# Kernel optimization log

Hardware: AMD Instinct MI355X
Metric: run time of the kernel (lower is better)

The kernel has to match this reference:

```python
import jax, jax.numpy as jnp
import numpy as np

PI = np.pi

def setup_inputs() -> dict:
    key = jax.random.key(0)
    ks = jax.random.split(key, 8)
    N, D, K, Q = 8192, 8, 64, 16
    return {
        "X": jax.random.normal(ks[0], (N, D), dtype=jnp.float32),
        "z": jax.random.normal(ks[1], (D, K, Q), dtype=jnp.float32),
        "weight": jax.random.uniform(ks[2], (Q,), dtype=jnp.float32) + 0.5,
        "mu": jax.random.uniform(ks[3], (D, Q), dtype=jnp.float32) + 0.5,
        "std": jax.random.uniform(ks[4], (D, Q), dtype=jnp.float32) + 0.5,
        "alpha": jax.random.uniform(ks[5], (K, Q), dtype=jnp.float32) * PI,
        "var_mu_w": 0.5 * jax.random.uniform(ks[6], (D, K, Q), dtype=jnp.float32),
        "var_sigma_w": 0.05 * jax.random.uniform(ks[7], (D, K, Q), dtype=jnp.float32),
    }

def reference(X, z, weight, mu, std, alpha, var_mu_w, var_sigma_w):
    # Faithful translation of vssgp.get_Ephi (Param.transform treated as identity)
    N, D = X.shape
    _, K, Q = z.shape
    two_over_K = 2.0 * weight[None, None, :] / K                 # [1,1,Q]
    mean_p = 1.0 / (mu + 1e-8)                                   # [D,Q]
    std_p = 1.0 / (2.0 * PI * std + 1e-8)                        # [D,Q]
    E_w = mean_p[:, None, :] + std_p[:, None, :] * var_mu_w      # [D,K,Q]
    xbar = 2.0 * PI * (X[:, :, None, None] - z[None])            # [N,D,K,Q]
    phase = jnp.einsum('ndkq,dkq->nkq', xbar, E_w)               # D-reduction
    cos_w = jnp.cos(alpha[None] + phase)                         # [N,K,Q]
    decay = jnp.exp(-0.5 * jnp.einsum(
        'ndkq,dkq->nkq', (std_p[None, :, None, :] * xbar) ** 2, var_sigma_w))
    E_phi = (jnp.sqrt(two_over_K) * decay * cos_w).reshape(N, K * Q)
    cos_2w = jnp.cos(2.0 * alpha[None] + 2.0 * phase)
    E_cos_sq = two_over_K * (0.5 + 0.5 * decay ** 4 * cos_2w)    # [N,K,Q]
    G = E_phi.T @ E_phi                                          # [KQ,KQ]
    diag_new = E_cos_sq.sum(axis=0).reshape(-1)
    G = G - jnp.diag(jnp.diag(G)) + jnp.diag(diag_new)
    return E_phi, G, E_cos_sq
```

## Files before the change

kernel.cpp:

```cpp
#include <hip/hip_runtime.h>

#define TWO_PI 6.2831853071795864769f

typedef float floatx4 __attribute__((ext_vector_type(4)));
typedef float f32x16 __attribute__((ext_vector_type(16)));
typedef __bf16 bf16x8 __attribute__((ext_vector_type(8)));

__device__ __forceinline__ unsigned short f32_to_bf16(float f) {
    unsigned int u = __float_as_uint(f);
    u += 0x7fffu + ((u >> 16) & 1u);
    return (unsigned short)(u >> 16);
}

__device__ __forceinline__ void gload_lds16(const void* g, void* l) {
    __builtin_amdgcn_global_load_lds(
        (__attribute__((address_space(1))) unsigned int*)g,
        (__attribute__((address_space(3))) unsigned int*)l, 16, 0, 0);
}

__global__ __launch_bounds__(256) void k_precompute(
    const float* __restrict__ z, const float* __restrict__ weight,
    const float* __restrict__ mu, const float* __restrict__ stdv,
    const float* __restrict__ alpha, const float* __restrict__ vmw,
    const float* __restrict__ vsw, float* __restrict__ coef,
    float* __restrict__ colsum)
{
    int kq = blockIdx.x * blockDim.x + threadIdx.x;
    if (kq >= 1024) return;
    colsum[kq] = 0.0f;
    int q = kq & 15;
    float w = weight[q];
    float t2k = w * (2.0f / 64.0f);
    float* c = coef + (size_t)kq * 32;
#pragma unroll
    for (int d = 0; d < 8; ++d) {
        float m = mu[d * 16 + q];
        float s = stdv[d * 16 + q];
        float mean_p = 1.0f / (m + 1e-8f);
        float std_p  = 1.0f / (TWO_PI * s + 1e-8f);
        float Ew  = mean_p + std_p * vmw[d * 1024 + kq];
        float sp2 = std_p * TWO_PI;
        c[d]      = TWO_PI * Ew;
        c[8 + d]  = sp2 * sp2 * vsw[d * 1024 + kq];
        c[16 + d] = z[d * 1024 + kq];
    }
    c[24] = alpha[kq];
    c[25] = sqrtf(t2k);
    c[26] = t2k;
}

__global__ __launch_bounds__(256) void k_ephi(
    const float* __restrict__ X, const float* __restrict__ coef,
    float* __restrict__ Ephi, float* __restrict__ Ecos,
    unsigned short* __restrict__ ET, float* __restrict__ colsum, int N)
{
    __shared__ float Xs[64][8];
    __shared__ unsigned short Ebf[64][66];
    __shared__ float red[256];

    const int tid = threadIdx.x;
    const int kq0 = blockIdx.x * 64;
    const int n0  = blockIdx.y * 64;

    for (int i = tid; i < 512; i += 256)
        Xs[i >> 3][i & 7] = X[(size_t)(n0 + (i >> 3)) * 8 + (i & 7)];
    __syncthreads();

    const int kql = tid & 63;
    const int kq  = kq0 + kql;
    const int nb  = (tid >> 6) * 16;

    const float* c = coef + (size_t)kq * 32;
    float Ac[8], u[8], zv[8];
    *(floatx4*)&Ac[0] = *(const floatx4*)(c + 0);
    *(floatx4*)&Ac[4] = *(const floatx4*)(c + 4);
    *(floatx4*)&u[0]  = *(const floatx4*)(c + 8);
    *(floatx4*)&u[4]  = *(const floatx4*)(c + 12);
    *(floatx4*)&zv[0] = *(const floatx4*)(c + 16);
    *(floatx4*)&zv[4] = *(const floatx4*)(c + 20);
    const float alp = c[24], sqw = c[25], t2k = c[26];

    float csum = 0.0f;
#pragma unroll 4
    for (int nl = 0; nl < 16; ++nl) {
        const int n = nb + nl;
        floatx4 xa = *(const floatx4*)&Xs[n][0];
        floatx4 xb = *(const floatx4*)&Xs[n][4];
        float ph = 0.0f, s = 0.0f;
#pragma unroll
        for (int d = 0; d < 4; ++d) {
            float t = xa[d] - zv[d];
            ph = fmaf(Ac[d], t, ph);
            s  = fmaf(u[d], t * t, s);
        }
#pragma unroll
        for (int d = 0; d < 4; ++d) {
            float t = xb[d] - zv[4 + d];
            ph = fmaf(Ac[4 + d], t, ph);
            s  = fmaf(u[4 + d], t * t, s);
        }
        float cw  = __cosf(alp + ph);
        float dec = __expf(-0.5f * s);
        float ep  = sqw * dec * cw;
        float d2  = dec * dec;
        float c2w = fmaf(2.0f * cw, cw, -1.0f);
        float ec  = t2k * fmaf(0.5f * d2 * d2, c2w, 0.5f);
        csum += ec;
        size_t idx = (size_t)(n0 + n) * 1024 + kq;
        Ephi[idx] = ep;
        Ecos[idx] = ec;
        Ebf[kql][n] = f32_to_bf16(ep);
    }
    red[tid] = csum;
    __syncthreads();
    if (tid < 64) {
        float v = red[tid] + red[tid + 64] + red[tid + 128] + red[tid + 192];
        atomicAdd(&colsum[kq0 + tid], v);
    }

    const int rw = tid >> 3;
    const int cw8 = tid & 7;
#pragma unroll
    for (int cc = 0; cc < 2; ++cc) {
        const int row = rw + cc * 32;
        const unsigned short* s8 = &Ebf[row][cw8 * 8];
        uint4 v;
        v.x = (unsigned)s8[0] | ((unsigned)s8[1] << 16);
        v.y = (unsigned)s8[2] | ((unsigned)s8[3] << 16);
        v.z = (unsigned)s8[4] | ((unsigned)s8[5] << 16);
        v.w = (unsigned)s8[6] | ((unsigned)s8[7] << 16);
        *(uint4*)&ET[(size_t)(kq0 + row) * N + n0 + cw8 * 8] = v;
    }
}

__global__ __launch_bounds__(256) void k_gemm(
    const unsigned short* __restrict__ ET, float* __restrict__ Gpart,
    int N, int KQ)
{
    __shared__ unsigned short At[2][128 * 64];
    __shared__ unsigned short Bt[2][128 * 64];

    const int tid  = threadIdx.x;
    const int wave = tid >> 6, lane = tid & 63;
    const int wi = wave >> 1, wj = wave & 1;

    const int bid = blockIdx.x;
    const int zc  = bid & 7;
    const int t8  = bid >> 3;
    const int i0  = (t8 >> 3) * 128;
    const int j0  = (t8 & 7) * 128;
    const int NS = N >> 3;
    const int nbase = zc * NS;
    const int nsteps = NS >> 6;

    const int srow = tid >> 3;
    const int sch  = (tid & 7) ^ (srow & 7);
    const size_t gA = (size_t)(i0 + srow) * N + nbase + sch * 8;
    const size_t gB = (size_t)(j0 + srow) * N + nbase + sch * 8;

    f32x16 acc[2][2] = {};

    auto STAGE = [&](int buf, int noff) {
        unsigned short* la = &At[buf][wave * 512];
        unsigned short* lb = &Bt[buf][wave * 512];
#pragma unroll
        for (int b = 0; b < 4; ++b) {
            gload_lds16(ET + gA + (size_t)(b * 32) * N + noff, la + b * 2048);
            gload_lds16(ET + gB + (size_t)(b * 32) * N + noff, lb + b * 2048);
        }
    };

    STAGE(0, 0);
    asm volatile("s_waitcnt vmcnt(0)" ::: "memory");
    __syncthreads();

    for (int t = 0; t < nsteps; ++t) {
        const int buf = t & 1;
        if (t + 1 < nsteps) STAGE(buf ^ 1, (t + 1) * 64);

        const unsigned short* Ab = &At[buf][0];
        const unsigned short* Bb = &Bt[buf][0];
        bf16x8 a[2][4], b[2][4];
#pragma unroll
        for (int m = 0; m < 2; ++m) {
            const int r = wi * 64 + m * 32 + (lane & 31);
#pragma unroll
            for (int ks = 0; ks < 4; ++ks) {
                const int ch = (ks * 2 + (lane >> 5)) ^ (r & 7);
                a[m][ks] = *(const bf16x8*)&Ab[r * 64 + ch * 8];
            }
        }
#pragma unroll
        for (int n = 0; n < 2; ++n) {
            const int r = wj * 64 + n * 32 + (lane & 31);
#pragma unroll
            for (int ks = 0; ks < 4; ++ks) {
                const int ch = (ks * 2 + (lane >> 5)) ^ (r & 7);
                b[n][ks] = *(const bf16x8*)&Bb[r * 64 + ch * 8];
            }
        }
#pragma unroll
        for (int ks = 0; ks < 4; ++ks)
#pragma unroll
            for (int m = 0; m < 2; ++m)
#pragma unroll
                for (int n = 0; n < 2; ++n)
                    acc[m][n] = __builtin_amdgcn_mfma_f32_32x32x16_bf16(
                        a[m][ks], b[n][ks], acc[m][n], 0, 0, 0);

        asm volatile("s_waitcnt vmcnt(0)" ::: "memory");
        __syncthreads();
    }

    float* Gp = Gpart + (size_t)zc * KQ * KQ;
    const int colb = j0 + wj * 64 + (lane & 31);
    const int rowb = i0 + wi * 64 + 4 * (lane >> 5);
#pragma unroll
    for (int m = 0; m < 2; ++m)
#pragma unroll
        for (int n = 0; n < 2; ++n)
#pragma unroll
            for (int reg = 0; reg < 16; ++reg) {
                const int row = rowb + m * 32 + (reg & 3) + 8 * (reg >> 2);
                Gp[(size_t)row * KQ + colb + n * 32] = acc[m][n][reg];
            }
}

__global__ __launch_bounds__(256) void k_reduce(
    const float* __restrict__ Gpart, const float* __restrict__ colsum,
    float* __restrict__ G, int KQ)
{
    const size_t off = ((size_t)blockIdx.x * 256 + threadIdx.x) * 4;
    const size_t stride = (size_t)KQ * KQ;
    floatx4 s = *(const floatx4*)&Gpart[off];
#pragma unroll
    for (int z = 1; z < 8; ++z)
        s += *(const floatx4*)&Gpart[(size_t)z * stride + off];
    const int row = (int)(off / (size_t)KQ);
    const int c0  = (int)(off % (size_t)KQ);
    if (row >= c0 && row < c0 + 4) s[row - c0] = colsum[row];
    *(floatx4*)&G[off] = s;
}

extern "C" void kernel_launch(void* const* d_in, const int* in_sizes, int n_in,
                              void* d_out, int out_size, void* d_ws, size_t ws_size,
                              hipStream_t stream)
{
    (void)n_in; (void)out_size; (void)ws_size;
    const float* X      = (const float*)d_in[0];
    const float* z      = (const float*)d_in[1];
    const float* weight = (const float*)d_in[2];
    const float* mu     = (const float*)d_in[3];
    const float* stdv   = (const float*)d_in[4];
    const float* alpha  = (const float*)d_in[5];
    const float* vmw    = (const float*)d_in[6];
    const float* vsw    = (const float*)d_in[7];

    const int N  = in_sizes[0] / 8;
    const int KQ = in_sizes[5];

    float* coef   = (float*)d_ws;
    float* colsum = (float*)((char*)d_ws + 131072);
    unsigned short* ET = (unsigned short*)((char*)d_ws + 135168);
    float* Gpart  = (float*)((char*)d_ws + 135168 + (size_t)KQ * N * 2);

    float* Ephi = (float*)d_out;
    float* G    = Ephi + (size_t)N * KQ;
    float* Ecos = G + (size_t)KQ * KQ;

    k_precompute<<<4, 256, 0, stream>>>(z, weight, mu, stdv, alpha, vmw, vsw, coef, colsum);
    k_ephi<<<dim3(KQ / 64, N / 64), 256, 0, stream>>>(X, coef, Ephi, Ecos, ET, colsum, N);
    k_gemm<<<512, 256, 0, stream>>>(ET, Gpart, N, KQ);
    k_reduce<<<(KQ * KQ) / 1024, 256, 0, stream>>>(Gpart, colsum, G, KQ);
}
```

Measured before the change: 148.6 us.

## Fuse coefficient precompute into ephi kernel, replace atomics with partials, prioritize MFMA

Removes the separate precompute kernel launch by having each ephi block compute its 64 columns of coefficients into shared memory. The column-sum atomics are replaced by per-block partial writes, which the reduce kernel sums serially for diagonal entries. MFMA sections in the GEMM are wrapped in s_setprio to raise wave priority. The cost is that coefficient work is recomputed across all 128 row-blocks, and the reduce kernel does a 128-iteration serial loop on diagonal threads.

New measurement: 168.4 us. 13.4% more time.

```diff
diff --git a/kernel.cpp b/kernel.cpp
--- a/kernel.cpp
+++ b/kernel.cpp
@@ -18,42 +18,15 @@
         (__attribute__((address_space(3))) unsigned int*)l, 16, 0, 0);
 }
 
-__global__ __launch_bounds__(256) void k_precompute(
-    const float* __restrict__ z, const float* __restrict__ weight,
-    const float* __restrict__ mu, const float* __restrict__ stdv,
-    const float* __restrict__ alpha, const float* __restrict__ vmw,
-    const float* __restrict__ vsw, float* __restrict__ coef,
-    float* __restrict__ colsum)
-{
-    int kq = blockIdx.x * blockDim.x + threadIdx.x;
-    if (kq >= 1024) return;
-    colsum[kq] = 0.0f;
-    int q = kq & 15;
-    float w = weight[q];
-    float t2k = w * (2.0f / 64.0f);
-    float* c = coef + (size_t)kq * 32;
-#pragma unroll
-    for (int d = 0; d < 8; ++d) {
-        float m = mu[d * 16 + q];
-        float s = stdv[d * 16 + q];
-        float mean_p = 1.0f / (m + 1e-8f);
-        float std_p  = 1.0f / (TWO_PI * s + 1e-8f);
-        float Ew  = mean_p + std_p * vmw[d * 1024 + kq];
-        float sp2 = std_p * TWO_PI;
-        c[d]      = TWO_PI * Ew;
-        c[8 + d]  = sp2 * sp2 * vsw[d * 1024 + kq];
-        c[16 + d] = z[d * 1024 + kq];
-    }
-    c[24] = alpha[kq];
-    c[25] = sqrtf(t2k);
-    c[26] = t2k;
-}
-
 __global__ __launch_bounds__(256) void k_ephi(
-    const float* __restrict__ X, const float* __restrict__ coef,
+    const float* __restrict__ X, const float* __restrict__ zc,
+    const float* __restrict__ weight, const float* __restrict__ mu,
+    const float* __restrict__ stdv, const float* __restrict__ alpha,
+    const float* __restrict__ vmw, const float* __restrict__ vsw,
     float* __restrict__ Ephi, float* __restrict__ Ecos,
-    unsigned short* __restrict__ ET, float* __restrict__ colsum, int N)
-{
+    unsigned short* __restrict__ ET, float* __restrict__ part, int N)
+{
+    __shared__ float cf[64][32];
     __shared__ float Xs[64][8];
     __shared__ unsigned short Ebf[64][66];
     __shared__ float red[256];
@@ -62,23 +35,46 @@
     const int kq0 = blockIdx.x * 64;
     const int n0  = blockIdx.y * 64;
 
-    for (int i = tid; i < 512; i += 256)
-        Xs[i >> 3][i & 7] = X[(size_t)(n0 + (i >> 3)) * 8 + (i & 7)];
+    {
+        int it = tid;
+#pragma unroll
+        for (int r = 0; r < 2; ++r, it += 256) {
+            const int kql = it >> 3, d = it & 7;
+            const int kq = kq0 + kql, q = kq & 15;
+            float m = mu[d * 16 + q];
+            float s = stdv[d * 16 + q];
+            float mean_p = 1.0f / (m + 1e-8f);
+            float std_p  = 1.0f / (TWO_PI * s + 1e-8f);
+            float Ew  = mean_p + std_p * vmw[d * 1024 + kq];
+            float sp2 = std_p * TWO_PI;
+            cf[kql][d]      = TWO_PI * Ew;
+            cf[kql][8 + d]  = sp2 * sp2 * vsw[d * 1024 + kq];
+            cf[kql][16 + d] = zc[d * 1024 + kq];
+        }
+        if (tid < 64) {
+            const int kq = kq0 + tid, q = kq & 15;
+            float t2k = weight[q] * (2.0f / 64.0f);
+            cf[tid][24] = alpha[kq];
+            cf[tid][25] = sqrtf(t2k);
+            cf[tid][26] = t2k;
+        }
+        for (int i = tid; i < 512; i += 256)
+            Xs[i >> 3][i & 7] = X[(size_t)(n0 + (i >> 3)) * 8 + (i & 7)];
+    }
     __syncthreads();
 
     const int kql = tid & 63;
     const int kq  = kq0 + kql;
     const int nb  = (tid >> 6) * 16;
 
-    const float* c = coef + (size_t)kq * 32;
     float Ac[8], u[8], zv[8];
-    *(floatx4*)&Ac[0] = *(const floatx4*)(c + 0);
-    *(floatx4*)&Ac[4] = *(const floatx4*)(c + 4);
-    *(floatx4*)&u[0]  = *(const floatx4*)(c + 8);
-    *(floatx4*)&u[4]  = *(const floatx4*)(c + 12);
-    *(floatx4*)&zv[0] = *(const floatx4*)(c + 16);
-    *(floatx4*)&zv[4] = *(const floatx4*)(c + 20);
-    const float alp = c[24], sqw = c[25], t2k = c[26];
+    *(floatx4*)&Ac[0] = *(const floatx4*)&cf[kql][0];
+    *(floatx4*)&Ac[4] = *(const floatx4*)&cf[kql][4];
+    *(floatx4*)&u[0]  = *(const floatx4*)&cf[kql][8];
+    *(floatx4*)&u[4]  = *(const floatx4*)&cf[kql][12];
+    *(floatx4*)&zv[0] = *(const floatx4*)&cf[kql][16];
+    *(floatx4*)&zv[4] = *(const floatx4*)&cf[kql][20];
+    const float alp = cf[kql][24], sqw = cf[kql][25], t2k = cf[kql][26];
 
     float csum = 0.0f;
 #pragma unroll 4
@@ -115,7 +111,7 @@
     __syncthreads();
     if (tid < 64) {
         float v = red[tid] + red[tid + 64] + red[tid + 128] + red[tid + 192];
-        atomicAdd(&colsum[kq0 + tid], v);
+        part[(size_t)blockIdx.y * 1024 + kq0 + tid] = v;
     }
 
     const int rw = tid >> 3;
@@ -199,6 +195,7 @@
                 b[n][ks] = *(const bf16x8*)&Bb[r * 64 + ch * 8];
             }
         }
+        __builtin_amdgcn_s_setprio(1);
 #pragma unroll
         for (int ks = 0; ks < 4; ++ks)
 #pragma unroll
@@ -207,6 +204,7 @@
                 for (int n = 0; n < 2; ++n)
                     acc[m][n] = __builtin_amdgcn_mfma_f32_32x32x16_bf16(
                         a[m][ks], b[n][ks], acc[m][n], 0, 0, 0);
+        __builtin_amdgcn_s_setprio(0);
 
         asm volatile("s_waitcnt vmcnt(0)" ::: "memory");
         __syncthreads();
@@ -227,8 +225,8 @@
 }
 
 __global__ __launch_bounds__(256) void k_reduce(
-    const float* __restrict__ Gpart, const float* __restrict__ colsum,
-    float* __restrict__ G, int KQ)
+    const float* __restrict__ Gpart, const float* __restrict__ part,
+    float* __restrict__ G, int KQ, int NB)
 {
     const size_t off = ((size_t)blockIdx.x * 256 + threadIdx.x) * 4;
     const size_t stride = (size_t)KQ * KQ;
@@ -238,7 +236,11 @@
         s += *(const floatx4*)&Gpart[(size_t)z * stride + off];
     const int row = (int)(off / (size_t)KQ);
     const int c0  = (int)(off % (size_t)KQ);
-    if (row >= c0 && row < c0 + 4) s[row - c0] = colsum[row];
+    if (row >= c0 && row < c0 + 4) {
+        float cs = 0.0f;
+        for (int i = 0; i < NB; ++i) cs += part[(size_t)i * KQ + row];
+        s[row - c0] = cs;
+    }
     *(floatx4*)&G[off] = s;
 }
 
@@ -258,18 +260,19 @@
 
     const int N  = in_sizes[0] / 8;
     const int KQ = in_sizes[5];
-
-    float* coef   = (float*)d_ws;
-    float* colsum = (float*)((char*)d_ws + 131072);
-    unsigned short* ET = (unsigned short*)((char*)d_ws + 135168);
-    float* Gpart  = (float*)((char*)d_ws + 135168 + (size_t)KQ * N * 2);
+    const int NB = N / 64;
+
+    unsigned short* ET = (unsigned short*)d_ws;
+    float* Gpart = (float*)((char*)d_ws + (size_t)KQ * N * 2);
+    float* part  = (float*)((char*)d_ws + (size_t)KQ * N * 2
+                            + 8ull * KQ * KQ * 4);
 
     float* Ephi = (float*)d_out;
     float* G    = Ephi + (size_t)N * KQ;
     float* Ecos = G + (size_t)KQ * KQ;
 
-    k_precompute<<<4, 256, 0, stream>>>(z, weight, mu, stdv, alpha, vmw, vsw, coef, colsum);
-    k_ephi<<<dim3(KQ / 64, N / 64), 256, 0, stream>>>(X, coef, Ephi, Ecos, ET, colsum, N);
+    k_ephi<<<dim3(KQ / 64, NB), 256, 0, stream>>>(
+        X, z, weight, mu, stdv, alpha, vmw, vsw, Ephi, Ecos, ET, part, N);
     k_gemm<<<512, 256, 0, stream>>>(ET, Gpart, N, KQ);
-    k_reduce<<<(KQ * KQ) / 1024, 256, 0, stream>>>(Gpart, colsum, G, KQ);
-}
+    k_reduce<<<(KQ * KQ) / 1024, 256, 0, stream>>>(Gpart, part, G, KQ, NB);
+}
```
